# Performance work log

Hardware: AMD Instinct MI355X
Metric: run time of the kernel (lower is better)

Reference implementation:

```python
import jax, jax.numpy as jnp
import numpy as np

N = 50000      # nodes
E = 800000     # edges (avg degree 16)
IN_DIM = 64
EMB = 64
L = 4          # num_layer
BN_EPS = 1e-5


def setup_inputs() -> dict:
    key = jax.random.key(0)
    ks = jax.random.split(key, 8)
    s = 0.05
    return {
        "x": jax.random.normal(ks[0], (N, 1, IN_DIM), jnp.float32),
        "edge_index": jax.random.randint(ks[1], (2, E), 0, N, jnp.int32),
        "edge_attr": jax.random.normal(ks[2], (E, 3), jnp.float32),
        "edge_weight": jax.random.uniform(ks[3], (E,), jnp.float32),
        # atom encoder Linear(in_dim, emb)
        "ae_w": jax.random.normal(ks[4], (IN_DIM, EMB), jnp.float32) * s,
        "ae_b": jnp.zeros((EMB,), jnp.float32),
        # per-layer GIN MLP: Linear -> BN -> ReLU -> Linear (stacked over L)
        "W1": jax.random.normal(ks[5], (L, EMB, EMB), jnp.float32) * s,
        "b1": jnp.zeros((L, EMB), jnp.float32),
        "g1": jnp.ones((L, EMB), jnp.float32),
        "be1": jnp.zeros((L, EMB), jnp.float32),
        "W2": jax.random.normal(ks[6], (L, EMB, EMB), jnp.float32) * s,
        "b2": jnp.zeros((L, EMB), jnp.float32),
        # outer per-layer BatchNorm1d in GNN_node
        "g_out": jnp.ones((L, EMB), jnp.float32),
        "be_out": jnp.zeros((L, EMB), jnp.float32),
    }


def _bn(h, g, b):
    # BatchNorm1d, training mode: batch stats over node dim, biased variance
    m = h.mean(0)
    v = h.var(0)
    return (h - m) * jax.lax.rsqrt(v + BN_EPS) * g + b


def reference(x, edge_index, edge_attr, edge_weight,
              ae_w, ae_b, W1, b1, g1, be1, W2, b2, g_out, be_out):
    # atom encoder on x[:, 0] : [N, in_dim] -> [N, emb]
    h = x[:, 0] @ ae_w + ae_b
    src = edge_index[0]
    dst = edge_index[1]
    n = h.shape[0]
    num_layers = W1.shape[0]
    for l in range(num_layers):
        # MyPyGINConv (train_eps=False, eps=0): scatter-add of x_j * w_e, plus self term
        msg = h[src] * edge_weight[:, None]                      # [E, emb]
        agg = jax.ops.segment_sum(msg, dst, num_segments=n)      # [N, emb]
        out = agg + h                                            # (1+eps)*x_r, eps=0
        # conv MLP: Linear -> BN -> ReLU -> Linear
        out = jax.nn.relu(_bn(out @ W1[l] + b1[l], g1[l], be1[l]))
        out = out @ W2[l] + b2[l]
        # outer BN + ReLU (always applied for 'originalgin'); dropout p=0; residual
        out = jax.nn.relu(_bn(out, g_out[l], be_out[l]))
        h = out + h
    return h  # JK='last'
```

## Files before the change

### kernel.cpp

```cpp
#include <hip/hip_runtime.h>
#include <stdint.h>

#define EMB 64
#define BN_EPS 1e-5f
#define BSH 8
#define CHUNK 4096
#define TS 68
#define NHB 120

typedef short bfrag __attribute__((ext_vector_type(8)));
typedef float f32x4 __attribute__((ext_vector_type(4)));

#define IN_F32    0
#define IN_BF16   1
#define IN_BF16BN 2

__device__ __forceinline__ unsigned short f2b(float x) {
    unsigned u = __float_as_uint(x);
    u += 0x7FFFu + ((u >> 16) & 1u);
    return (unsigned short)(u >> 16);
}
__device__ __forceinline__ float b2f(unsigned short v) {
    return __uint_as_float(((unsigned)v) << 16);
}

__global__ void __launch_bounds__(256) k_prep_hist(
        const float* __restrict__ ae_w, const float* __restrict__ W1,
        const float* __restrict__ W2, unsigned short* __restrict__ Wt16,
        int* __restrict__ hist_part, float* __restrict__ stats,
        const int* __restrict__ ei, int E, int L, int nstats) {
    __shared__ int lh[256];
    const int tid = threadIdx.x;
    const int nw = (1 + 2 * L) * EMB * EMB;
    for (int gid = blockIdx.x * 256 + tid; gid < nw; gid += gridDim.x * 256) {
        int m = gid >> 12;
        int j = (gid >> 6) & 63;
        int k = gid & 63;
        const float* src = (m == 0) ? ae_w
                         : (m <= L ? W1 + (size_t)(m - 1) * EMB * EMB
                                   : W2 + (size_t)(m - 1 - L) * EMB * EMB);
        Wt16[gid] = f2b(src[k * EMB + j]);
    }
    for (int i = blockIdx.x * 256 + tid; i < nstats; i += gridDim.x * 256)
        stats[i] = 0.0f;
    if (blockIdx.x < NHB) {
        lh[tid] = 0;
        __syncthreads();
        for (int e = blockIdx.x * 256 + tid; e < E; e += NHB * 256)
            atomicAdd(&lh[((unsigned)ei[E + e]) >> BSH], 1);
        __syncthreads();
        hist_part[blockIdx.x * 256 + tid] = lh[tid];
    }
}

__global__ void __launch_bounds__(256) k_bscan(const int* __restrict__ hist_part,
                                               int* __restrict__ bbase,
                                               int* __restrict__ bcur, int nb) {
    __shared__ int a[256];
    const int t = threadIdx.x;
    int v = 0;
    for (int b = 0; b < NHB; b++) v += hist_part[b * 256 + t];
    a[t] = v;
    __syncthreads();
    for (int off = 1; off < 256; off <<= 1) {
        int x = (t >= off) ? a[t - off] : 0;
        __syncthreads();
        a[t] += x;
        __syncthreads();
    }
    int excl = a[t] - v;
    if (t < nb) { bbase[t] = excl; bcur[t] = excl; }
    if (t == nb - 1) bbase[nb] = a[t];
}

__global__ void __launch_bounds__(256) k_part(
        const int* __restrict__ ei, const float* __restrict__ ew,
        int* __restrict__ bcur, int2* __restrict__ eG, int E) {
    __shared__ int lcnt[256], lbase[256], loff[256];
    const int tid = threadIdx.x;
    const int c0 = blockIdx.x * CHUNK;
    lcnt[tid] = 0;
    __syncthreads();
    int src[16], pk[16], g[16];
    float wt[16];
#pragma unroll
    for (int i = 0; i < 16; i++) {
        int e = c0 + i * 256 + tid;
        if (e < E) {
            int d = ei[E + e];
            src[i] = ei[e];
            wt[i] = ew[e];
            g[i] = ((unsigned)d) >> BSH;
            pk[i] = src[i] | ((d & 255) << 24);
            atomicAdd(&lcnt[g[i]], 1);
        } else g[i] = -1;
    }
    __syncthreads();
    if (lcnt[tid]) lbase[tid] = atomicAdd(&bcur[tid], lcnt[tid]);
    loff[tid] = 0;
    __syncthreads();
#pragma unroll
    for (int i = 0; i < 16; i++) {
        if (g[i] >= 0) {
            int pos = lbase[g[i]] + atomicAdd(&loff[g[i]], 1);
            eG[pos] = make_int2(pk[i], __float_as_int(wt[i]));
        }
    }
}

__global__ void __launch_bounds__(256) k_build(
        const int2* __restrict__ eG, const int* __restrict__ bbase,
        int* __restrict__ rowst, int* __restrict__ counts,
        int2* __restrict__ pairs, int N) {
    __shared__ int lcnt[256], a[256], lcur[256];
    const int t = threadIdx.x;
    const int b = blockIdx.x;
    const int e0 = bbase[b], e1 = bbase[b + 1];
    lcnt[t] = 0;
    __syncthreads();
    for (int i = e0 + t; i < e1; i += 256)
        atomicAdd(&lcnt[((unsigned)eG[i].x) >> 24], 1);
    __syncthreads();
    int v = lcnt[t];
    a[t] = v;
    __syncthreads();
    for (int off = 1; off < 256; off <<= 1) {
        int x = (t >= off) ? a[t - off] : 0;
        __syncthreads();
        a[t] += x;
        __syncthreads();
    }
    int excl = a[t] - v;
    lcur[t] = excl;
    int node = (b << BSH) + t;
    if (node < N) { rowst[node] = e0 + excl; counts[node] = v; }
    __syncthreads();
    for (int i = e0 + t; i < e1; i += 256) {
        int2 p = eG[i];
        int loc = ((unsigned)p.x) >> 24;
        int pos = e0 + atomicAdd(&lcur[loc], 1);
        pairs[pos] = make_int2(p.x & 0x00FFFFFF, p.y);
    }
}

__global__ void k_agg(const unsigned short* __restrict__ hb,
                      const int* __restrict__ rowst,
                      const int* __restrict__ counts, const int2* __restrict__ pairs,
                      unsigned short* __restrict__ out16, int N) {
    const int lane = threadIdx.x & 63;
    int wave = (blockIdx.x * blockDim.x + threadIdx.x) >> 6;
    const int nwaves = (gridDim.x * blockDim.x) >> 6;
    for (int nA = wave; nA < N; nA += 2 * nwaves) {
        const int nB = nA + nwaves;
        const int uA = __builtin_amdgcn_readfirstlane(nA);
        const int uB = __builtin_amdgcn_readfirstlane(nB);
        const bool hasB = uB < N;
        int sA = rowst[uA], eA = sA + counts[uA];
        int sB = 0, eB = 0;
        if (hasB) { sB = rowst[uB]; eB = sB + counts[uB]; }
        float aA[8] = {0, 0, 0, 0, 0, 0, 0, 0};
        float aB[8] = {0, 0, 0, 0, 0, 0, 0, 0};
        for (int xA = sA, xB = sB; (xA < eA) | (xB < eB); xA += 8, xB += 8) {
            int2 pA[8], pB[8];
            float wA[8], wB[8];
#pragma unroll
            for (int k = 0; k < 8; k++) {
                int i = xA + k;
                bool ok = i < eA;
                int2 p = pairs[ok ? i : 0];
                pA[k] = p;
                wA[k] = ok ? __int_as_float(p.y) : 0.f;
            }
#pragma unroll
            for (int k = 0; k < 8; k++) {
                int i = xB + k;
                bool ok = i < eB;
                int2 p = pairs[ok ? i : 0];
                pB[k] = p;
                wB[k] = ok ? __int_as_float(p.y) : 0.f;
            }
#pragma unroll
            for (int k = 0; k < 8; k++)
                aA[k] = fmaf(wA[k], b2f(hb[(size_t)pA[k].x * EMB + lane]), aA[k]);
#pragma unroll
            for (int k = 0; k < 8; k++)
                aB[k] = fmaf(wB[k], b2f(hb[(size_t)pB[k].x * EMB + lane]), aB[k]);
        }
        float sumA = (((aA[0] + aA[1]) + (aA[2] + aA[3])) +
                      ((aA[4] + aA[5]) + (aA[6] + aA[7]))) +
                     b2f(hb[(size_t)uA * EMB + lane]);
        out16[(size_t)uA * EMB + lane] = f2b(sumA);
        if (hasB) {
            float sumB = (((aB[0] + aB[1]) + (aB[2] + aB[3])) +
                          ((aB[4] + aB[5]) + (aB[6] + aB[7]))) +
                         b2f(hb[(size_t)uB * EMB + lane]);
            out16[(size_t)uB * EMB + lane] = f2b(sumB);
        }
    }
}

template <int INMODE, bool DO_STATS>
__global__ void __launch_bounds__(256) k_mmx(
        const void* __restrict__ in_v, const unsigned short* __restrict__ Wt,
        const float* __restrict__ bias, const float* __restrict__ stats,
        const float* __restrict__ g, const float* __restrict__ be, float invN,
        unsigned short* __restrict__ out16, float* __restrict__ st_out, int N) {
    __shared__ float tb[64 * TS];
    __shared__ float st_part[128];
    __shared__ float scs[EMB], shs[EMB];
    const int tid = threadIdx.x;
    const int lane = tid & 63;
    const int wv = tid >> 6;
    const int node0 = blockIdx.x * 64;
    const int m = lane & 15;
    const int quad = lane >> 4;

    if (DO_STATS && tid < 128) st_part[tid] = 0.f;
    if (INMODE == IN_BF16BN) {
        if (tid < EMB) {
            float s1 = 0.f, s2 = 0.f;
#pragma unroll
            for (int k = 0; k < 8; k++) {
                s1 += stats[k * 128 + tid];
                s2 += stats[k * 128 + 64 + tid];
            }
            float mm = s1 * invN;
            float va = fmaf(s2, invN, -mm * mm);
            float rs = rsqrtf(va + BN_EPS);
            float sc = rs * g[tid];
            scs[tid] = sc;
            shs[tid] = fmaf(-mm, sc, be[tid]);
        }
        __syncthreads();
    }

    const int arow = node0 + wv * 16 + m;
    bfrag a0 = {0, 0, 0, 0, 0, 0, 0, 0}, a1 = {0, 0, 0, 0, 0, 0, 0, 0};
    if (arow < N) {
        if (INMODE == IN_BF16) {
            const unsigned short* ab =
                (const unsigned short*)in_v + (size_t)arow * EMB + quad * 8;
            a0 = *(const bfrag*)ab;
            a1 = *(const bfrag*)(ab + 32);
        } else if (INMODE == IN_BF16BN) {
            const unsigned short* ab =
                (const unsigned short*)in_v + (size_t)arow * EMB + quad * 8;
            bfrag r0 = *(const bfrag*)ab;
            bfrag r1 = *(const bfrag*)(ab + 32);
#pragma unroll
            for (int j = 0; j < 8; j++) {
                int k0 = quad * 8 + j;
                float v0 = b2f((unsigned short)r0[j]);
                float v1 = b2f((unsigned short)r1[j]);
                v0 = fmaxf(0.f, fmaf(v0, scs[k0], shs[k0]));
                v1 = fmaxf(0.f, fmaf(v1, scs[k0 + 32], shs[k0 + 32]));
                a0[j] = (short)f2b(v0);
                a1[j] = (short)f2b(v1);
            }
        } else {
            const float* af = (const float*)in_v + (size_t)arow * EMB + quad * 8;
#pragma unroll
            for (int j = 0; j < 8; j++) {
                a0[j] = (short)f2b(af[j]);
                a1[j] = (short)f2b(af[32 + j]);
            }
        }
    }

    const unsigned short* bb = Wt + (size_t)m * EMB + quad * 8;
    f32x4 acc[4];
#pragma unroll
    for (int c = 0; c < 4; c++) {
        bfrag b0 = *(const bfrag*)(bb + c * 16 * EMB);
        bfrag b1 = *(const bfrag*)(bb + c * 16 * EMB + 32);
        f32x4 z = {0.f, 0.f, 0.f, 0.f};
        z = __builtin_amdgcn_mfma_f32_16x16x32_bf16(a0, b0, z, 0, 0, 0);
        z = __builtin_amdgcn_mfma_f32_16x16x32_bf16(a1, b1, z, 0, 0, 0);
        acc[c] = z;
    }

#pragma unroll
    for (int c = 0; c < 4; c++) {
        float bj = bias[c * 16 + m];
#pragma unroll
        for (int r = 0; r < 4; r++) {
            int row = wv * 16 + quad * 4 + r;
            float v = (node0 + row < N) ? (acc[c][r] + bj) : 0.f;
            tb[row * TS + c * 16 + m] = v;
        }
    }
    __syncthreads();

    if (DO_STATS) {
        float ssum = 0.f, ssq = 0.f;
#pragma unroll
        for (int i = 0; i < 16; i++) {
            float v = tb[(wv * 16 + i) * TS + lane];
            ssum += v;
            ssq = fmaf(v, v, ssq);
        }
        atomicAdd(&st_part[lane], ssum);
        atomicAdd(&st_part[64 + lane], ssq);
    }

    ushort4* o4 = (ushort4*)(out16 + (size_t)node0 * EMB);
#pragma unroll
    for (int it = 0; it < 4; it++) {
        int flat4 = it * 256 + tid;
        int nsub = flat4 >> 4;
        int c4 = flat4 & 15;
        if (node0 + nsub < N) {
            const float* s4 = tb + nsub * TS + c4 * 4;
            ushort4 o;
            o.x = f2b(s4[0]); o.y = f2b(s4[1]);
            o.z = f2b(s4[2]); o.w = f2b(s4[3]);
            o4[flat4] = o;
        }
    }

    if (DO_STATS) {
        __syncthreads();
        if (tid < 128)
            atomicAdd(&st_out[((unsigned)blockIdx.x & 7u) * 128 + tid], st_part[tid]);
    }
}

template <bool LAST>
__global__ void k_bnres(const unsigned short* __restrict__ u16,
                        const float* __restrict__ st,
                        const float* __restrict__ g, const float* __restrict__ be,
                        unsigned short* __restrict__ hb16, float* __restrict__ out32,
                        float invN, int total4) {
    __shared__ float scs[EMB], shs[EMB];
    const int tid = threadIdx.x;
    if (tid < EMB) {
        float s1 = 0.f, s2 = 0.f;
#pragma unroll
        for (int k = 0; k < 8; k++) {
            s1 += st[k * 128 + tid];
            s2 += st[k * 128 + 64 + tid];
        }
        float mm = s1 * invN;
        float va = fmaf(s2, invN, -mm * mm);
        float rs = rsqrtf(va + BN_EPS);
        float sc = rs * g[tid];
        scs[tid] = sc;
        shs[tid] = fmaf(-mm, sc, be[tid]);
    }
    __syncthreads();
    int stride = gridDim.x * blockDim.x;
    for (int i4 = blockIdx.x * blockDim.x + tid; i4 < total4; i4 += stride) {
        int c4 = i4 & 15;
        ushort4 uv = ((const ushort4*)u16)[i4];
        ushort4 hv = ((const ushort4*)hb16)[i4];
        float4 scv = *(const float4*)&scs[c4 * 4];
        float4 shv = *(const float4*)&shs[c4 * 4];
        float4 o;
        o.x = fmaxf(0.f, fmaf(b2f(uv.x), scv.x, shv.x)) + b2f(hv.x);
        o.y = fmaxf(0.f, fmaf(b2f(uv.y), scv.y, shv.y)) + b2f(hv.y);
        o.z = fmaxf(0.f, fmaf(b2f(uv.z), scv.z, shv.z)) + b2f(hv.z);
        o.w = fmaxf(0.f, fmaf(b2f(uv.w), scv.w, shv.w)) + b2f(hv.w);
        if (LAST) {
            ((float4*)out32)[i4] = o;
        } else {
            ushort4 ob;
            ob.x = f2b(o.x); ob.y = f2b(o.y);
            ob.z = f2b(o.z); ob.w = f2b(o.w);
            ((ushort4*)hb16)[i4] = ob;
        }
    }
}

extern "C" void kernel_launch(void* const* d_in, const int* in_sizes, int n_in,
                              void* d_out, int out_size, void* d_ws, size_t ws_size,
                              hipStream_t stream) {
    const float* x     = (const float*)d_in[0];
    const int*   ei    = (const int*)d_in[1];
    const float* ew    = (const float*)d_in[3];
    const float* ae_w  = (const float*)d_in[4];
    const float* ae_b  = (const float*)d_in[5];
    const float* W1    = (const float*)d_in[6];
    const float* b1    = (const float*)d_in[7];
    const float* g1    = (const float*)d_in[8];
    const float* be1   = (const float*)d_in[9];
    const float* W2    = (const float*)d_in[10];
    const float* b2    = (const float*)d_in[11];
    const float* g_out = (const float*)d_in[12];
    const float* be_out= (const float*)d_in[13];

    const int N = in_sizes[0] / EMB;
    const int E = in_sizes[3];
    const int L = in_sizes[6] / (EMB * EMB);
    const float invN = 1.0f / (float)N;
    const int NBUCK = (N + 255) >> BSH;

    uintptr_t p = (uintptr_t)d_ws;
    auto alloc = [&](size_t bytes) -> void* {
        p = (p + 255) & ~(uintptr_t)255;
        void* r = (void*)p;
        p += bytes;
        return r;
    };
    unsigned short* hb16 = (unsigned short*)alloc((size_t)N * EMB * 2);
    unsigned short* b16a = (unsigned short*)alloc((size_t)N * EMB * 2);
    unsigned short* t16  = (unsigned short*)alloc((size_t)N * EMB * 2);
    unsigned short* Wt16 = (unsigned short*)alloc((size_t)(1 + 2 * L) * EMB * EMB * 2);
    int*   counts= (int*)alloc((size_t)N * 4);
    int*   rowst = (int*)alloc((size_t)N * 4);
    int*   hist_part = (int*)alloc((size_t)NHB * 256 * 4);
    int*   bbase = (int*)alloc(257 * 4);
    int*   bcur  = (int*)alloc(256 * 4);
    int2*  pairs = (int2*)alloc((size_t)E * 8);
    int2*  eG    = (int2*)alloc((size_t)E * 8);
    float* stats = (float*)alloc((size_t)L * 2 * 8 * 128 * 4);
    (void)ws_size; (void)n_in; (void)out_size;

    const int nw = (1 + 2 * L) * EMB * EMB;
    const int nstats = L * 2 * 8 * 128;
    const int nprep = (nw + 255) / 256;
    hipLaunchKernelGGL(k_prep_hist, dim3(nprep > NHB ? nprep : NHB), dim3(256), 0,
                       stream, ae_w, W1, W2, Wt16, hist_part, stats, ei, E, L, nstats);

    const int ntiles = (N + 63) / 64;
    hipLaunchKernelGGL((k_mmx<IN_F32, false>), dim3(ntiles), dim3(256), 0, stream,
                       x, Wt16, ae_b, (const float*)nullptr, (const float*)nullptr,
                       (const float*)nullptr, 0.f, hb16, (float*)nullptr, N);

    hipLaunchKernelGGL(k_bscan, dim3(1), dim3(256), 0, stream,
                       hist_part, bbase, bcur, NBUCK);
    hipLaunchKernelGGL(k_part, dim3((E + CHUNK - 1) / CHUNK), dim3(256), 0, stream,
                       ei, ew, bcur, eG, E);
    hipLaunchKernelGGL(k_build, dim3(NBUCK), dim3(256), 0, stream,
                       eG, bbase, rowst, counts, pairs, N);

    for (int l = 0; l < L; l++) {
        float* stats1 = stats + (size_t)(l * 2 + 0) * 1024;
        float* stats2 = stats + (size_t)(l * 2 + 1) * 1024;

        hipLaunchKernelGGL(k_agg, dim3(2048), dim3(256), 0, stream,
                           hb16, rowst, counts, pairs, b16a, N);
        hipLaunchKernelGGL((k_mmx<IN_BF16, true>), dim3(ntiles), dim3(256), 0, stream,
                           b16a, Wt16 + (size_t)(1 + l) * EMB * EMB, b1 + (size_t)l * EMB,
                           (const float*)nullptr, (const float*)nullptr,
                           (const float*)nullptr, 0.f, t16, stats1, N);
        hipLaunchKernelGGL((k_mmx<IN_BF16BN, true>), dim3(ntiles), dim3(256), 0, stream,
                           t16, Wt16 + (size_t)(1 + L + l) * EMB * EMB, b2 + (size_t)l * EMB,
                           stats1, g1 + (size_t)l * EMB, be1 + (size_t)l * EMB, invN,
                           b16a, stats2, N);
        if (l == L - 1) {
            hipLaunchKernelGGL((k_bnres<true>), dim3(1024), dim3(256), 0, stream,
                               b16a, stats2, g_out + (size_t)l * EMB,
                               be_out + (size_t)l * EMB, hb16, (float*)d_out,
                               invN, N * 16);
        } else {
            hipLaunchKernelGGL((k_bnres<false>), dim3(1024), dim3(256), 0, stream,
                               b16a, stats2, g_out + (size_t)l * EMB,
                               be_out + (size_t)l * EMB, hb16, (float*)nullptr,
                               invN, N * 16);
        }
    }
}
```

Before: 403.7 us.

## Fuse neighbor aggregation into first GEMM and merge encoder with CSR build

Each 64-node tile now computes its own aggregation (gather of bf16 neighbor features plus self term) straight into shared memory, then feeds the first MFMA GEMM from LDS. This removes the separate k_agg kernel and the bf16 round trip of the aggregated tensor through global memory on every layer. The atom-encoder GEMM is also merged into the CSR build kernel as extra blocks, so one launch does both and they can overlap. The trade-off is that aggregation parallelism is now fixed to one tile per block (4 waves, 16 nodes each), which could lower occupancy or latency hiding for the irregular gathers compared with the former grid-stride layout.

```diff
diff --git a/kernel.cpp b/kernel.cpp
--- a/kernel.cpp
+++ b/kernel.cpp
@@ -6,22 +6,30 @@
 #define BSH 8
 #define CHUNK 4096
 #define TS 68
+#define ALS 72
 #define NHB 120
 
 typedef short bfrag __attribute__((ext_vector_type(8)));
 typedef float f32x4 __attribute__((ext_vector_type(4)));
 
 #define IN_F32    0
-#define IN_BF16   1
 #define IN_BF16BN 2
+#define IN_AGG    3
+
+struct SMM {
+  float tb[64 * TS];
+  float st[128];
+  float scs[EMB], shs[EMB];
+  unsigned short aL[64 * ALS];
+};
 
 __device__ __forceinline__ unsigned short f2b(float x) {
-    unsigned u = __float_as_uint(x);
-    u += 0x7FFFu + ((u >> 16) & 1u);
-    return (unsigned short)(u >> 16);
+  unsigned u = __float_as_uint(x);
+  u += 0x7FFFu + ((u >> 16) & 1u);
+  return (unsigned short)(u >> 16);
 }
 __device__ __forceinline__ float b2f(unsigned short v) {
-    return __uint_as_float(((unsigned)v) << 16);
+  return __uint_as_float(((unsigned)v) << 16);
 }
 
 __global__ void __launch_bounds__(256) k_prep_hist(
@@ -29,300 +37,324 @@
         const float* __restrict__ W2, unsigned short* __restrict__ Wt16,
         int* __restrict__ hist_part, float* __restrict__ stats,
         const int* __restrict__ ei, int E, int L, int nstats) {
-    __shared__ int lh[256];
-    const int tid = threadIdx.x;
-    const int nw = (1 + 2 * L) * EMB * EMB;
-    for (int gid = blockIdx.x * 256 + tid; gid < nw; gid += gridDim.x * 256) {
-        int m = gid >> 12;
-        int j = (gid >> 6) & 63;
-        int k = gid & 63;
-        const float* src = (m == 0) ? ae_w
-                         : (m <= L ? W1 + (size_t)(m - 1) * EMB * EMB
-                                   : W2 + (size_t)(m - 1 - L) * EMB * EMB);
-        Wt16[gid] = f2b(src[k * EMB + j]);
-    }
-    for (int i = blockIdx.x * 256 + tid; i < nstats; i += gridDim.x * 256)
-        stats[i] = 0.0f;
-    if (blockIdx.x < NHB) {
-        lh[tid] = 0;
-        __syncthreads();
-        for (int e = blockIdx.x * 256 + tid; e < E; e += NHB * 256)
-            atomicAdd(&lh[((unsigned)ei[E + e]) >> BSH], 1);
-        __syncthreads();
-        hist_part[blockIdx.x * 256 + tid] = lh[tid];
-    }
+  __shared__ int lh[256];
+  const int tid = threadIdx.x;
+  const int nw = (1 + 2 * L) * EMB * EMB;
+  for (int gid = blockIdx.x * 256 + tid; gid < nw; gid += gridDim.x * 256) {
+    int m = gid >> 12;
+    int j = (gid >> 6) & 63;
+    int k = gid & 63;
+    const float* src = (m == 0) ? ae_w
+                     : (m <= L ? W1 + (size_t)(m - 1) * EMB * EMB
+                               : W2 + (size_t)(m - 1 - L) * EMB * EMB);
+    Wt16[gid] = f2b(src[k * EMB + j]);
+  }
+  for (int i = blockIdx.x * 256 + tid; i < nstats; i += gridDim.x * 256)
+    stats[i] = 0.0f;
+  if (blockIdx.x < NHB) {
+    lh[tid] = 0;
+    __syncthreads();
+    for (int e = blockIdx.x * 256 + tid; e < E; e += NHB * 256)
+      atomicAdd(&lh[((unsigned)ei[E + e]) >> BSH], 1);
+    __syncthreads();
+    hist_part[blockIdx.x * 256 + tid] = lh[tid];
+  }
 }
 
 __global__ void __launch_bounds__(256) k_bscan(const int* __restrict__ hist_part,
                                                int* __restrict__ bbase,
                                                int* __restrict__ bcur, int nb) {
-    __shared__ int a[256];
-    const int t = threadIdx.x;
-    int v = 0;
-    for (int b = 0; b < NHB; b++) v += hist_part[b * 256 + t];
-    a[t] = v;
-    __syncthreads();
-    for (int off = 1; off < 256; off <<= 1) {
-        int x = (t >= off) ? a[t - off] : 0;
-        __syncthreads();
-        a[t] += x;
-        __syncthreads();
-    }
-    int excl = a[t] - v;
-    if (t < nb) { bbase[t] = excl; bcur[t] = excl; }
-    if (t == nb - 1) bbase[nb] = a[t];
+  __shared__ int a[256];
+  const int t = threadIdx.x;
+  int v = 0;
+  for (int b = 0; b < NHB; b++) v += hist_part[b * 256 + t];
+  a[t] = v;
+  __syncthreads();
+  for (int off = 1; off < 256; off <<= 1) {
+    int x = (t >= off) ? a[t - off] : 0;
+    __syncthreads();
+    a[t] += x;
+    __syncthreads();
+  }
+  int excl = a[t] - v;
+  if (t < nb) { bbase[t] = excl; bcur[t] = excl; }
+  if (t == nb - 1) bbase[nb] = a[t];
 }
 
 __global__ void __launch_bounds__(256) k_part(
         const int* __restrict__ ei, const float* __restrict__ ew,
         int* __restrict__ bcur, int2* __restrict__ eG, int E) {
-    __shared__ int lcnt[256], lbase[256], loff[256];
-    const int tid = threadIdx.x;
-    const int c0 = blockIdx.x * CHUNK;
-    lcnt[tid] = 0;
-    __syncthreads();
-    int src[16], pk[16], g[16];
-    float wt[16];
+  __shared__ int lcnt[256], lbase[256], loff[256];
+  const int tid = threadIdx.x;
+  const int c0 = blockIdx.x * CHUNK;
+  lcnt[tid] = 0;
+  __syncthreads();
+  int src[16], pk[16], g[16];
+  float wt[16];
+#pragma unroll
+  for (int i = 0; i < 16; i++) {
+    int e = c0 + i * 256 + tid;
+    if (e < E) {
+      int d = ei[E + e];
+      src[i] = ei[e];
+      wt[i] = ew[e];
+      g[i] = ((unsigned)d) >> BSH;
+      pk[i] = src[i] | ((d & 255) << 24);
+      atomicAdd(&lcnt[g[i]], 1);
+    } else g[i] = -1;
+  }
+  __syncthreads();
+  if (lcnt[tid]) lbase[tid] = atomicAdd(&bcur[tid], lcnt[tid]);
+  loff[tid] = 0;
+  __syncthreads();
+#pragma unroll
+  for (int i = 0; i < 16; i++) {
+    if (g[i] >= 0) {
+      int pos = lbase[g[i]] + atomicAdd(&loff[g[i]], 1);
+      eG[pos] = make_int2(pk[i], __float_as_int(wt[i]));
+    }
+  }
+}
+
+template <int INMODE, bool DO_STATS>
+__device__ __forceinline__ void mm_tile(SMM& sm, int tile,
+    const void* in_v, const unsigned short* Wt, const float* bias,
+    const float* stats_in, const float* g, const float* be, float invN,
+    unsigned short* out16, float* st_out,
+    const unsigned short* hb, const int* rowst, const int* counts,
+    const int2* pairs, int N) {
+  const int tid = threadIdx.x;
+  const int lane = tid & 63;
+  const int wv = tid >> 6;
+  const int node0 = tile * 64;
+  const int m = lane & 15;
+  const int quad = lane >> 4;
+
+  if (DO_STATS && tid < 128) sm.st[tid] = 0.f;
+  if (INMODE == IN_BF16BN && tid < EMB) {
+    float s1 = 0.f, s2 = 0.f;
+#pragma unroll
+    for (int k = 0; k < 8; k++) {
+      s1 += stats_in[k * 128 + tid];
+      s2 += stats_in[k * 128 + 64 + tid];
+    }
+    float mu = s1 * invN;
+    float va = fmaf(s2, invN, -mu * mu);
+    float rs = rsqrtf(va + BN_EPS);
+    float sc = rs * g[tid];
+    sm.scs[tid] = sc;
+    sm.shs[tid] = fmaf(-mu, sc, be[tid]);
+  }
+  if (INMODE == IN_AGG) {
+#pragma unroll 1
+    for (int i = 0; i < 16; i += 2) {
+      const int rA = wv * 16 + i;
+      const int nA = node0 + rA, nB = nA + 1;
+      int sA = 0, eA = 0, sB = 0, eB = 0;
+      if (nA < N) { sA = rowst[nA]; eA = sA + counts[nA]; }
+      if (nB < N) { sB = rowst[nB]; eB = sB + counts[nB]; }
+      float accA[8] = {0, 0, 0, 0, 0, 0, 0, 0};
+      float accB[8] = {0, 0, 0, 0, 0, 0, 0, 0};
+      for (int xA = sA, xB = sB; (xA < eA) | (xB < eB); xA += 8, xB += 8) {
+        int2 pA[8], pB[8];
+        float wA[8], wB[8];
+#pragma unroll
+        for (int k2 = 0; k2 < 8; k2++) {
+          int ia = xA + k2;
+          bool oa = ia < eA;
+          int2 p = pairs[oa ? ia : 0];
+          pA[k2] = p;
+          wA[k2] = oa ? __int_as_float(p.y) : 0.f;
+        }
+#pragma unroll
+        for (int k2 = 0; k2 < 8; k2++) {
+          int ib = xB + k2;
+          bool ob = ib < eB;
+          int2 p = pairs[ob ? ib : 0];
+          pB[k2] = p;
+          wB[k2] = ob ? __int_as_float(p.y) : 0.f;
+        }
+#pragma unroll
+        for (int k2 = 0; k2 < 8; k2++)
+          accA[k2] = fmaf(wA[k2], b2f(hb[(size_t)pA[k2].x * EMB + lane]), accA[k2]);
+#pragma unroll
+        for (int k2 = 0; k2 < 8; k2++)
+          accB[k2] = fmaf(wB[k2], b2f(hb[(size_t)pB[k2].x * EMB + lane]), accB[k2]);
+      }
+      float sA8 = (((accA[0] + accA[1]) + (accA[2] + accA[3])) +
+                   ((accA[4] + accA[5]) + (accA[6] + accA[7])));
+      float sB8 = (((accB[0] + accB[1]) + (accB[2] + accB[3])) +
+                   ((accB[4] + accB[5]) + (accB[6] + accB[7])));
+      if (nA < N) sA8 += b2f(hb[(size_t)nA * EMB + lane]);
+      if (nB < N) sB8 += b2f(hb[(size_t)nB * EMB + lane]);
+      sm.aL[rA * ALS + lane] = f2b(nA < N ? sA8 : 0.f);
+      sm.aL[(rA + 1) * ALS + lane] = f2b(nB < N ? sB8 : 0.f);
+    }
+  }
+  if (INMODE == IN_BF16BN || INMODE == IN_AGG || DO_STATS)
+    __syncthreads();
+
+  bfrag a0 = {0, 0, 0, 0, 0, 0, 0, 0}, a1 = {0, 0, 0, 0, 0, 0, 0, 0};
+  if (INMODE == IN_AGG) {
+    const unsigned short* ab = &sm.aL[(wv * 16 + m) * ALS + quad * 8];
+    a0 = *(const bfrag*)ab;
+    a1 = *(const bfrag*)(ab + 32);
+  } else {
+    const int arow = node0 + wv * 16 + m;
+    if (arow < N) {
+      if (INMODE == IN_BF16BN) {
+        const unsigned short* ab =
+            (const unsigned short*)in_v + (size_t)arow * EMB + quad * 8;
+        bfrag r0 = *(const bfrag*)ab;
+        bfrag r1 = *(const bfrag*)(ab + 32);
+#pragma unroll
+        for (int j = 0; j < 8; j++) {
+          int k0 = quad * 8 + j;
+          float v0 = b2f((unsigned short)r0[j]);
+          float v1 = b2f((unsigned short)r1[j]);
+          v0 = fmaxf(0.f, fmaf(v0, sm.scs[k0], sm.shs[k0]));
+          v1 = fmaxf(0.f, fmaf(v1, sm.scs[k0 + 32], sm.shs[k0 + 32]));
+          a0[j] = (short)f2b(v0);
+          a1[j] = (short)f2b(v1);
+        }
+      } else {
+        const float* af = (const float*)in_v + (size_t)arow * EMB + quad * 8;
+#pragma unroll
+        for (int j = 0; j < 8; j++) {
+          a0[j] = (short)f2b(af[j]);
+          a1[j] = (short)f2b(af[32 + j]);
+        }
+      }
+    }
+  }
+
+  const unsigned short* bb = Wt + (size_t)m * EMB + quad * 8;
+  f32x4 acc[4];
+#pragma unroll
+  for (int c = 0; c < 4; c++) {
+    bfrag b0 = *(const bfrag*)(bb + c * 16 * EMB);
+    bfrag b1 = *(const bfrag*)(bb + c * 16 * EMB + 32);
+    f32x4 z = {0.f, 0.f, 0.f, 0.f};
+    z = __builtin_amdgcn_mfma_f32_16x16x32_bf16(a0, b0, z, 0, 0, 0);
+    z = __builtin_amdgcn_mfma_f32_16x16x32_bf16(a1, b1, z, 0, 0, 0);
+    acc[c] = z;
+  }
+
+#pragma unroll
+  for (int c = 0; c < 4; c++) {
+    float bj = bias[c * 16 + m];
+#pragma unroll
+    for (int r = 0; r < 4; r++) {
+      int row = wv * 16 + quad * 4 + r;
+      float v = (node0 + row < N) ? (acc[c][r] + bj) : 0.f;
+      sm.tb[row * TS + c * 16 + m] = v;
+    }
+  }
+  __syncthreads();
+
+  if (DO_STATS) {
+    float ssum = 0.f, ssq = 0.f;
 #pragma unroll
     for (int i = 0; i < 16; i++) {
-        int e = c0 + i * 256 + tid;
-        if (e < E) {
-            int d = ei[E + e];
-            src[i] = ei[e];
-            wt[i] = ew[e];
-            g[i] = ((unsigned)d) >> BSH;
-            pk[i] = src[i] | ((d & 255) << 24);
-            atomicAdd(&lcnt[g[i]], 1);
-        } else g[i] = -1;
-    }
-    __syncthreads();
-    if (lcnt[tid]) lbase[tid] = atomicAdd(&bcur[tid], lcnt[tid]);
-    loff[tid] = 0;
-    __syncthreads();
-#pragma unroll
-    for (int i = 0; i < 16; i++) {
-        if (g[i] >= 0) {
-            int pos = lbase[g[i]] + atomicAdd(&loff[g[i]], 1);
-            eG[pos] = make_int2(pk[i], __float_as_int(wt[i]));
-        }
-    }
-}
-
-__global__ void __launch_bounds__(256) k_build(
+      float v = sm.tb[(wv * 16 + i) * TS + lane];
+      ssum += v;
+      ssq = fmaf(v, v, ssq);
+    }
+    atomicAdd(&sm.st[lane], ssum);
+    atomicAdd(&sm.st[64 + lane], ssq);
+  }
+
+  ushort4* o4 = (ushort4*)(out16 + (size_t)node0 * EMB);
+#pragma unroll
+  for (int it = 0; it < 4; it++) {
+    int flat4 = it * 256 + tid;
+    int nsub = flat4 >> 4;
+    int c4 = flat4 & 15;
+    if (node0 + nsub < N) {
+      const float* s4 = sm.tb + nsub * TS + c4 * 4;
+      ushort4 o;
+      o.x = f2b(s4[0]); o.y = f2b(s4[1]);
+      o.z = f2b(s4[2]); o.w = f2b(s4[3]);
+      o4[flat4] = o;
+    }
+  }
+
+  if (DO_STATS) {
+    __syncthreads();
+    if (tid < 128)
+      atomicAdd(&st_out[((unsigned)tile & 7u) * 128 + tid], sm.st[tid]);
+  }
+}
+
+__global__ void __launch_bounds__(256) k_build_enc(
         const int2* __restrict__ eG, const int* __restrict__ bbase,
         int* __restrict__ rowst, int* __restrict__ counts,
-        int2* __restrict__ pairs, int N) {
-    __shared__ int lcnt[256], a[256], lcur[256];
-    const int t = threadIdx.x;
-    const int b = blockIdx.x;
-    const int e0 = bbase[b], e1 = bbase[b + 1];
-    lcnt[t] = 0;
-    __syncthreads();
-    for (int i = e0 + t; i < e1; i += 256)
-        atomicAdd(&lcnt[((unsigned)eG[i].x) >> 24], 1);
-    __syncthreads();
-    int v = lcnt[t];
-    a[t] = v;
-    __syncthreads();
-    for (int off = 1; off < 256; off <<= 1) {
-        int x = (t >= off) ? a[t - off] : 0;
-        __syncthreads();
-        a[t] += x;
-        __syncthreads();
-    }
-    int excl = a[t] - v;
-    lcur[t] = excl;
-    int node = (b << BSH) + t;
-    if (node < N) { rowst[node] = e0 + excl; counts[node] = v; }
-    __syncthreads();
-    for (int i = e0 + t; i < e1; i += 256) {
-        int2 p = eG[i];
-        int loc = ((unsigned)p.x) >> 24;
-        int pos = e0 + atomicAdd(&lcur[loc], 1);
-        pairs[pos] = make_int2(p.x & 0x00FFFFFF, p.y);
-    }
-}
-
-__global__ void k_agg(const unsigned short* __restrict__ hb,
-                      const int* __restrict__ rowst,
-                      const int* __restrict__ counts, const int2* __restrict__ pairs,
-                      unsigned short* __restrict__ out16, int N) {
-    const int lane = threadIdx.x & 63;
-    int wave = (blockIdx.x * blockDim.x + threadIdx.x) >> 6;
-    const int nwaves = (gridDim.x * blockDim.x) >> 6;
-    for (int nA = wave; nA < N; nA += 2 * nwaves) {
-        const int nB = nA + nwaves;
-        const int uA = __builtin_amdgcn_readfirstlane(nA);
-        const int uB = __builtin_amdgcn_readfirstlane(nB);
-        const bool hasB = uB < N;
-        int sA = rowst[uA], eA = sA + counts[uA];
-        int sB = 0, eB = 0;
-        if (hasB) { sB = rowst[uB]; eB = sB + counts[uB]; }
-        float aA[8] = {0, 0, 0, 0, 0, 0, 0, 0};
-        float aB[8] = {0, 0, 0, 0, 0, 0, 0, 0};
-        for (int xA = sA, xB = sB; (xA < eA) | (xB < eB); xA += 8, xB += 8) {
-            int2 pA[8], pB[8];
-            float wA[8], wB[8];
-#pragma unroll
-            for (int k = 0; k < 8; k++) {
-                int i = xA + k;
-                bool ok = i < eA;
-                int2 p = pairs[ok ? i : 0];
-                pA[k] = p;
-                wA[k] = ok ? __int_as_float(p.y) : 0.f;
-            }
-#pragma unroll
-            for (int k = 0; k < 8; k++) {
-                int i = xB + k;
-                bool ok = i < eB;
-                int2 p = pairs[ok ? i : 0];
-                pB[k] = p;
-                wB[k] = ok ? __int_as_float(p.y) : 0.f;
-            }
-#pragma unroll
-            for (int k = 0; k < 8; k++)
-                aA[k] = fmaf(wA[k], b2f(hb[(size_t)pA[k].x * EMB + lane]), aA[k]);
-#pragma unroll
-            for (int k = 0; k < 8; k++)
-                aB[k] = fmaf(wB[k], b2f(hb[(size_t)pB[k].x * EMB + lane]), aB[k]);
-        }
-        float sumA = (((aA[0] + aA[1]) + (aA[2] + aA[3])) +
-                      ((aA[4] + aA[5]) + (aA[6] + aA[7]))) +
-                     b2f(hb[(size_t)uA * EMB + lane]);
-        out16[(size_t)uA * EMB + lane] = f2b(sumA);
-        if (hasB) {
-            float sumB = (((aB[0] + aB[1]) + (aB[2] + aB[3])) +
-                          ((aB[4] + aB[5]) + (aB[6] + aB[7]))) +
-                         b2f(hb[(size_t)uB * EMB + lane]);
-            out16[(size_t)uB * EMB + lane] = f2b(sumB);
-        }
-    }
-}
-
-template <int INMODE, bool DO_STATS>
-__global__ void __launch_bounds__(256) k_mmx(
-        const void* __restrict__ in_v, const unsigned short* __restrict__ Wt,
-        const float* __restrict__ bias, const float* __restrict__ stats,
-        const float* __restrict__ g, const float* __restrict__ be, float invN,
+        int2* __restrict__ pairs, int nbuck,
+        const float* __restrict__ x, const unsigned short* __restrict__ Wt16,
+        const float* __restrict__ ae_b, unsigned short* __restrict__ hb16,
+        int N) {
+  __shared__ union {
+    SMM mm;
+    struct { int lcnt[256]; int a[256]; int lcur[256]; } bld;
+  } u;
+  if ((int)blockIdx.x >= nbuck) {
+    mm_tile<IN_F32, false>(u.mm, blockIdx.x - nbuck, x, Wt16, ae_b,
+                           nullptr, nullptr, nullptr, 0.f, hb16, nullptr,
+                           nullptr, nullptr, nullptr, nullptr, N);
+    return;
+  }
+  const int t = threadIdx.x;
+  const int b = blockIdx.x;
+  const int e0 = bbase[b], e1 = bbase[b + 1];
+  u.bld.lcnt[t] = 0;
+  __syncthreads();
+  for (int i = e0 + t; i < e1; i += 256)
+    atomicAdd(&u.bld.lcnt[((unsigned)eG[i].x) >> 24], 1);
+  __syncthreads();
+  int v = u.bld.lcnt[t];
+  u.bld.a[t] = v;
+  __syncthreads();
+  for (int off = 1; off < 256; off <<= 1) {
+    int x2 = (t >= off) ? u.bld.a[t - off] : 0;
+    __syncthreads();
+    u.bld.a[t] += x2;
+    __syncthreads();
+  }
+  int excl = u.bld.a[t] - v;
+  u.bld.lcur[t] = excl;
+  int node = (b << BSH) + t;
+  if (node < N) { rowst[node] = e0 + excl; counts[node] = v; }
+  __syncthreads();
+  for (int i = e0 + t; i < e1; i += 256) {
+    int2 p = eG[i];
+    int loc = ((unsigned)p.x) >> 24;
+    int pos = e0 + atomicAdd(&u.bld.lcur[loc], 1);
+    pairs[pos] = make_int2(p.x & 0x00FFFFFF, p.y);
+  }
+}
+
+__global__ void __launch_bounds__(256) k_mmagg(
+        const unsigned short* __restrict__ hb,
+        const int* __restrict__ rowst, const int* __restrict__ counts,
+        const int2* __restrict__ pairs,
+        const unsigned short* __restrict__ Wt, const float* __restrict__ bias,
         unsigned short* __restrict__ out16, float* __restrict__ st_out, int N) {
-    __shared__ float tb[64 * TS];
-    __shared__ float st_part[128];
-    __shared__ float scs[EMB], shs[EMB];
-    const int tid = threadIdx.x;
-    const int lane = tid & 63;
-    const int wv = tid >> 6;
-    const int node0 = blockIdx.x * 64;
-    const int m = lane & 15;
-    const int quad = lane >> 4;
-
-    if (DO_STATS && tid < 128) st_part[tid] = 0.f;
-    if (INMODE == IN_BF16BN) {
-        if (tid < EMB) {
-            float s1 = 0.f, s2 = 0.f;
-#pragma unroll
-            for (int k = 0; k < 8; k++) {
-                s1 += stats[k * 128 + tid];
-                s2 += stats[k * 128 + 64 + tid];
-            }
-            float mm = s1 * invN;
-            float va = fmaf(s2, invN, -mm * mm);
-            float rs = rsqrtf(va + BN_EPS);
-            float sc = rs * g[tid];
-            scs[tid] = sc;
-            shs[tid] = fmaf(-mm, sc, be[tid]);
-        }
-        __syncthreads();
-    }
-
-    const int arow = node0 + wv * 16 + m;
-    bfrag a0 = {0, 0, 0, 0, 0, 0, 0, 0}, a1 = {0, 0, 0, 0, 0, 0, 0, 0};
-    if (arow < N) {
-        if (INMODE == IN_BF16) {
-            const unsigned short* ab =
-                (const unsigned short*)in_v + (size_t)arow * EMB + quad * 8;
-            a0 = *(const bfrag*)ab;
-            a1 = *(const bfrag*)(ab + 32);
-        } else if (INMODE == IN_BF16BN) {
-            const unsigned short* ab =
-                (const unsigned short*)in_v + (size_t)arow * EMB + quad * 8;
-            bfrag r0 = *(const bfrag*)ab;
-            bfrag r1 = *(const bfrag*)(ab + 32);
-#pragma unroll
-            for (int j = 0; j < 8; j++) {
-                int k0 = quad * 8 + j;
-                float v0 = b2f((unsigned short)r0[j]);
-                float v1 = b2f((unsigned short)r1[j]);
-                v0 = fmaxf(0.f, fmaf(v0, scs[k0], shs[k0]));
-                v1 = fmaxf(0.f, fmaf(v1, scs[k0 + 32], shs[k0 + 32]));
-                a0[j] = (short)f2b(v0);
-                a1[j] = (short)f2b(v1);
-            }
-        } else {
-            const float* af = (const float*)in_v + (size_t)arow * EMB + quad * 8;
-#pragma unroll
-            for (int j = 0; j < 8; j++) {
-                a0[j] = (short)f2b(af[j]);
-                a1[j] = (short)f2b(af[32 + j]);
-            }
-        }
-    }
-
-    const unsigned short* bb = Wt + (size_t)m * EMB + quad * 8;
-    f32x4 acc[4];
-#pragma unroll
-    for (int c = 0; c < 4; c++) {
-        bfrag b0 = *(const bfrag*)(bb + c * 16 * EMB);
-        bfrag b1 = *(const bfrag*)(bb + c * 16 * EMB + 32);
-        f32x4 z = {0.f, 0.f, 0.f, 0.f};
-        z = __builtin_amdgcn_mfma_f32_16x16x32_bf16(a0, b0, z, 0, 0, 0);
-        z = __builtin_amdgcn_mfma_f32_16x16x32_bf16(a1, b1, z, 0, 0, 0);
-        acc[c] = z;
-    }
-
-#pragma unroll
-    for (int c = 0; c < 4; c++) {
-        float bj = bias[c * 16 + m];
-#pragma unroll
-        for (int r = 0; r < 4; r++) {
-            int row = wv * 16 + quad * 4 + r;
-            float v = (node0 + row < N) ? (acc[c][r] + bj) : 0.f;
-            tb[row * TS + c * 16 + m] = v;
-        }
-    }
-    __syncthreads();
-
-    if (DO_STATS) {
-        float ssum = 0.f, ssq = 0.f;
-#pragma unroll
-        for (int i = 0; i < 16; i++) {
-            float v = tb[(wv * 16 + i) * TS + lane];
-            ssum += v;
-            ssq = fmaf(v, v, ssq);
-        }
-        atomicAdd(&st_part[lane], ssum);
-        atomicAdd(&st_part[64 + lane], ssq);
-    }
-
-    ushort4* o4 = (ushort4*)(out16 + (size_t)node0 * EMB);
-#pragma unroll
-    for (int it = 0; it < 4; it++) {
-        int flat4 = it * 256 + tid;
-        int nsub = flat4 >> 4;
-        int c4 = flat4 & 15;
-        if (node0 + nsub < N) {
-            const float* s4 = tb + nsub * TS + c4 * 4;
-            ushort4 o;
-            o.x = f2b(s4[0]); o.y = f2b(s4[1]);
-            o.z = f2b(s4[2]); o.w = f2b(s4[3]);
-            o4[flat4] = o;
-        }
-    }
-
-    if (DO_STATS) {
-        __syncthreads();
-        if (tid < 128)
-            atomicAdd(&st_out[((unsigned)blockIdx.x & 7u) * 128 + tid], st_part[tid]);
-    }
+  __shared__ SMM sm;
+  mm_tile<IN_AGG, true>(sm, blockIdx.x, nullptr, Wt, bias, nullptr, nullptr,
+                        nullptr, 0.f, out16, st_out, hb, rowst, counts,
+                        pairs, N);
+}
+
+__global__ void __launch_bounds__(256) k_mm2(
+        const unsigned short* __restrict__ in16,
+        const unsigned short* __restrict__ Wt, const float* __restrict__ bias,
+        const float* __restrict__ stats_in, const float* __restrict__ g,
+        const float* __restrict__ be, float invN,
+        unsigned short* __restrict__ out16, float* __restrict__ st_out, int N) {
+  __shared__ SMM sm;
+  mm_tile<IN_BF16BN, true>(sm, blockIdx.x, in16, Wt, bias, stats_in, g, be,
+                           invN, out16, st_out, nullptr, nullptr, nullptr,
+                           nullptr, N);
 }
 
 template <bool LAST>
@@ -331,132 +363,127 @@
                         const float* __restrict__ g, const float* __restrict__ be,
                         unsigned short* __restrict__ hb16, float* __restrict__ out32,
                         float invN, int total4) {
-    __shared__ float scs[EMB], shs[EMB];
-    const int tid = threadIdx.x;
-    if (tid < EMB) {
-        float s1 = 0.f, s2 = 0.f;
-#pragma unroll
-        for (int k = 0; k < 8; k++) {
-            s1 += st[k * 128 + tid];
-            s2 += st[k * 128 + 64 + tid];
-        }
-        float mm = s1 * invN;
-        float va = fmaf(s2, invN, -mm * mm);
-        float rs = rsqrtf(va + BN_EPS);
-        float sc = rs * g[tid];
-        scs[tid] = sc;
-        shs[tid] = fmaf(-mm, sc, be[tid]);
-    }
-    __syncthreads();
-    int stride = gridDim.x * blockDim.x;
-    for (int i4 = blockIdx.x * blockDim.x + tid; i4 < total4; i4 += stride) {
-        int c4 = i4 & 15;
-        ushort4 uv = ((const ushort4*)u16)[i4];
-        ushort4 hv = ((const ushort4*)hb16)[i4];
-        float4 scv = *(const float4*)&scs[c4 * 4];
-        float4 shv = *(const float4*)&shs[c4 * 4];
-        float4 o;
-        o.x = fmaxf(0.f, fmaf(b2f(uv.x), scv.x, shv.x)) + b2f(hv.x);
-        o.y = fmaxf(0.f, fmaf(b2f(uv.y), scv.y, shv.y)) + b2f(hv.y);
-        o.z = fmaxf(0.f, fmaf(b2f(uv.z), scv.z, shv.z)) + b2f(hv.z);
-        o.w = fmaxf(0.f, fmaf(b2f(uv.w), scv.w, shv.w)) + b2f(hv.w);
-        if (LAST) {
-            ((float4*)out32)[i4] = o;
-        } else {
-            ushort4 ob;
-            ob.x = f2b(o.x); ob.y = f2b(o.y);
-            ob.z = f2b(o.z); ob.w = f2b(o.w);
-            ((ushort4*)hb16)[i4] = ob;
-        }
-    }
+  __shared__ float scs[EMB], shs[EMB];
+  const int tid = threadIdx.x;
+  if (tid < EMB) {
+    float s1 = 0.f, s2 = 0.f;
+#pragma unroll
+    for (int k = 0; k < 8; k++) {
+      s1 += st[k * 128 + tid];
+      s2 += st[k * 128 + 64 + tid];
+    }
+    float mm = s1 * invN;
+    float va = fmaf(s2, invN, -mm * mm);
+    float rs = rsqrtf(va + BN_EPS);
+    float sc = rs * g[tid];
+    scs[tid] = sc;
+    shs[tid] = fmaf(-mm, sc, be[tid]);
+  }
+  __syncthreads();
+  int stride = gridDim.x * blockDim.x;
+  for (int i4 = blockIdx.x * blockDim.x + tid; i4 < total4; i4 += stride) {
+    int c4 = i4 & 15;
+    ushort4 uv = ((const ushort4*)u16)[i4];
+    ushort4 hv = ((const ushort4*)hb16)[i4];
+    float4 scv = *(const float4*)&scs[c4 * 4];
+    float4 shv = *(const float4*)&shs[c4 * 4];
+    float4 o;
+    o.x = fmaxf(0.f, fmaf(b2f(uv.x), scv.x, shv.x)) + b2f(hv.x);
+    o.y = fmaxf(0.f, fmaf(b2f(uv.y), scv.y, shv.y)) + b2f(hv.y);
+    o.z = fmaxf(0.f, fmaf(b2f(uv.z), scv.z, shv.z)) + b2f(hv.z);
+    o.w = fmaxf(0.f, fmaf(b2f(uv.w), scv.w, shv.w)) + b2f(hv.w);
+    if (LAST) {
+      ((float4*)out32)[i4] = o;
+    } else {
+      ushort4 ob;
+      ob.x = f2b(o.x); ob.y = f2b(o.y);
+      ob.z = f2b(o.z); ob.w = f2b(o.w);
+      ((ushort4*)hb16)[i4] = ob;
+    }
+  }
 }
 
 extern "C" void kernel_launch(void* const* d_in, const int* in_sizes, int n_in,
                               void* d_out, int out_size, void* d_ws, size_t ws_size,
                               hipStream_t stream) {
-    const float* x     = (const float*)d_in[0];
-    const int*   ei    = (const int*)d_in[1];
-    const float* ew    = (const float*)d_in[3];
-    const float* ae_w  = (const float*)d_in[4];
-    const float* ae_b  = (const float*)d_in[5];
-    const float* W1    = (const float*)d_in[6];
-    const float* b1    = (const float*)d_in[7];
-    const float* g1    = (const float*)d_in[8];
-    const float* be1   = (const float*)d_in[9];
-    const float* W2    = (const float*)d_in[10];
-    const float* b2    = (const float*)d_in[11];
-    const float* g_out = (const float*)d_in[12];
-    const float* be_out= (const float*)d_in[13];
-
-    const int N = in_sizes[0] / EMB;
-    const int E = in_sizes[3];
-    const int L = in_sizes[6] / (EMB * EMB);
-    const float invN = 1.0f / (float)N;
-    const int NBUCK = (N + 255) >> BSH;
-
-    uintptr_t p = (uintptr_t)d_ws;
-    auto alloc = [&](size_t bytes) -> void* {
-        p = (p + 255) & ~(uintptr_t)255;
-        void* r = (void*)p;
-        p += bytes;
-        return r;
-    };
-    unsigned short* hb16 = (unsigned short*)alloc((size_t)N * EMB * 2);
-    unsigned short* b16a = (unsigned short*)alloc((size_t)N * EMB * 2);
-    unsigned short* t16  = (unsigned short*)alloc((size_t)N * EMB * 2);
-    unsigned short* Wt16 = (unsigned short*)alloc((size_t)(1 + 2 * L) * EMB * EMB * 2);
-    int*   counts= (int*)alloc((size_t)N * 4);
-    int*   rowst = (int*)alloc((size_t)N * 4);
-    int*   hist_part = (int*)alloc((size_t)NHB * 256 * 4);
-    int*   bbase = (int*)alloc(257 * 4);
-    int*   bcur  = (int*)alloc(256 * 4);
-    int2*  pairs = (int2*)alloc((size_t)E * 8);
-    int2*  eG    = (int2*)alloc((size_t)E * 8);
-    float* stats = (float*)alloc((size_t)L * 2 * 8 * 128 * 4);
-    (void)ws_size; (void)n_in; (void)out_size;
-
-    const int nw = (1 + 2 * L) * EMB * EMB;
-    const int nstats = L * 2 * 8 * 128;
-    const int nprep = (nw + 255) / 256;
-    hipLaunchKernelGGL(k_prep_hist, dim3(nprep > NHB ? nprep : NHB), dim3(256), 0,
-                       stream, ae_w, W1, W2, Wt16, hist_part, stats, ei, E, L, nstats);
-
-    const int ntiles = (N + 63) / 64;
-    hipLaunchKernelGGL((k_mmx<IN_F32, false>), dim3(ntiles), dim3(256), 0, stream,
-                       x, Wt16, ae_b, (const float*)nullptr, (const float*)nullptr,
-                       (const float*)nullptr, 0.f, hb16, (float*)nullptr, N);
-
-    hipLaunchKernelGGL(k_bscan, dim3(1), dim3(256), 0, stream,
-                       hist_part, bbase, bcur, NBUCK);
-    hipLaunchKernelGGL(k_part, dim3((E + CHUNK - 1) / CHUNK), dim3(256), 0, stream,
-                       ei, ew, bcur, eG, E);
-    hipLaunchKernelGGL(k_build, dim3(NBUCK), dim3(256), 0, stream,
-                       eG, bbase, rowst, counts, pairs, N);
-
-    for (int l = 0; l < L; l++) {
-        float* stats1 = stats + (size_t)(l * 2 + 0) * 1024;
-        float* stats2 = stats + (size_t)(l * 2 + 1) * 1024;
-
-        hipLaunchKernelGGL(k_agg, dim3(2048), dim3(256), 0, stream,
-                           hb16, rowst, counts, pairs, b16a, N);
-        hipLaunchKernelGGL((k_mmx<IN_BF16, true>), dim3(ntiles), dim3(256), 0, stream,
-                           b16a, Wt16 + (size_t)(1 + l) * EMB * EMB, b1 + (size_t)l * EMB,
-                           (const float*)nullptr, (const float*)nullptr,
-                           (const float*)nullptr, 0.f, t16, stats1, N);
-        hipLaunchKernelGGL((k_mmx<IN_BF16BN, true>), dim3(ntiles), dim3(256), 0, stream,
-                           t16, Wt16 + (size_t)(1 + L + l) * EMB * EMB, b2 + (size_t)l * EMB,
-                           stats1, g1 + (size_t)l * EMB, be1 + (size_t)l * EMB, invN,
-                           b16a, stats2, N);
-        if (l == L - 1) {
-            hipLaunchKernelGGL((k_bnres<true>), dim3(1024), dim3(256), 0, stream,
-                               b16a, stats2, g_out + (size_t)l * EMB,
-                               be_out + (size_t)l * EMB, hb16, (float*)d_out,
-                               invN, N * 16);
-        } else {
-            hipLaunchKernelGGL((k_bnres<false>), dim3(1024), dim3(256), 0, stream,
-                               b16a, stats2, g_out + (size_t)l * EMB,
-                               be_out + (size_t)l * EMB, hb16, (float*)nullptr,
-                               invN, N * 16);
-        }
-    }
-}
+  const float* x     = (const float*)d_in[0];
+  const int*   ei    = (const int*)d_in[1];
+  const float* ew    = (const float*)d_in[3];
+  const float* ae_w  = (const float*)d_in[4];
+  const float* ae_b  = (const float*)d_in[5];
+  const float* W1    = (const float*)d_in[6];
+  const float* b1    = (const float*)d_in[7];
+  const float* g1    = (const float*)d_in[8];
+  const float* be1   = (const float*)d_in[9];
+  const float* W2    = (const float*)d_in[10];
+  const float* b2    = (const float*)d_in[11];
+  const float* g_out = (const float*)d_in[12];
+  const float* be_out= (const float*)d_in[13];
+
+  const int N = in_sizes[0] / EMB;
+  const int E = in_sizes[3];
+  const int L = in_sizes[6] / (EMB * EMB);
+  const float invN = 1.0f / (float)N;
+  const int NBUCK = (N + 255) >> BSH;
+
+  uintptr_t p = (uintptr_t)d_ws;
+  auto alloc = [&](size_t bytes) -> void* {
+    p = (p + 255) & ~(uintptr_t)255;
+    void* r = (void*)p;
+    p += bytes;
+    return r;
+  };
+  unsigned short* hb16 = (unsigned short*)alloc((size_t)N * EMB * 2);
+  unsigned short* b16a = (unsigned short*)alloc((size_t)N * EMB * 2);
+  unsigned short* t16  = (unsigned short*)alloc((size_t)N * EMB * 2);
+  unsigned short* Wt16 = (unsigned short*)alloc((size_t)(1 + 2 * L) * EMB * EMB * 2);
+  int*   counts= (int*)alloc((size_t)N * 4);
+  int*   rowst = (int*)alloc((size_t)N * 4);
+  int*   hist_part = (int*)alloc((size_t)NHB * 256 * 4);
+  int*   bbase = (int*)alloc(257 * 4);
+  int*   bcur  = (int*)alloc(256 * 4);
+  int2*  pairs = (int2*)alloc((size_t)E * 8);
+  int2*  eG    = (int2*)alloc((size_t)E * 8);
+  float* stats = (float*)alloc((size_t)L * 2 * 8 * 128 * 4);
+  (void)ws_size; (void)n_in; (void)out_size;
+
+  const int nw = (1 + 2 * L) * EMB * EMB;
+  const int nstats = L * 2 * 8 * 128;
+  const int nprep = (nw + 255) / 256;
+  hipLaunchKernelGGL(k_prep_hist, dim3(nprep > NHB ? nprep : NHB), dim3(256), 0,
+                     stream, ae_w, W1, W2, Wt16, hist_part, stats, ei, E, L, nstats);
+
+  const int ntiles = (N + 63) / 64;
+  hipLaunchKernelGGL(k_bscan, dim3(1), dim3(256), 0, stream,
+                     hist_part, bbase, bcur, NBUCK);
+  hipLaunchKernelGGL(k_part, dim3((E + CHUNK - 1) / CHUNK), dim3(256), 0, stream,
+                     ei, ew, bcur, eG, E);
+  hipLaunchKernelGGL(k_build_enc, dim3(NBUCK + ntiles), dim3(256), 0, stream,
+                     eG, bbase, rowst, counts, pairs, NBUCK,
+                     x, Wt16, ae_b, hb16, N);
+
+  for (int l = 0; l < L; l++) {
+    float* stats1 = stats + (size_t)(l * 2 + 0) * 1024;
+    float* stats2 = stats + (size_t)(l * 2 + 1) * 1024;
+
+    hipLaunchKernelGGL(k_mmagg, dim3(ntiles), dim3(256), 0, stream,
+                       hb16, rowst, counts, pairs,
+                       Wt16 + (size_t)(1 + l) * EMB * EMB, b1 + (size_t)l * EMB,
+                       t16, stats1, N);
+    hipLaunchKernelGGL(k_mm2, dim3(ntiles), dim3(256), 0, stream,
+                       t16, Wt16 + (size_t)(1 + L + l) * EMB * EMB,
+                       b2 + (size_t)l * EMB, stats1, g1 + (size_t)l * EMB,
+                       be1 + (size_t)l * EMB, invN, b16a, stats2, N);
+    if (l == L - 1) {
+      hipLaunchKernelGGL((k_bnres<true>), dim3(1024), dim3(256), 0, stream,
+                         b16a, stats2, g_out + (size_t)l * EMB,
+                         be_out + (size_t)l * EMB, hb16, (float*)d_out,
+                         invN, N * 16);
+    } else {
+      hipLaunchKernelGGL((k_bnres<false>), dim3(1024), dim3(256), 0, stream,
+                         b16a, stats2, g_out + (size_t)l * EMB,
+                         be_out + (size_t)l * EMB, hb16, (float*)nullptr,
+                         invN, N * 16);
+    }
+  }
+}
```

Result: slower. 474.2 us (+17.4%).
